# Kernel optimization log

Hardware: AMD Instinct MI355X
Metric: run time of the kernel (lower is better)

The kernel has to match this reference:

```python
import jax, jax.numpy as jnp
import numpy as np

B, S, H, KVH, D = 1, 2048, 32, 8, 128
ROPE_THETA = 500000.0


def _rotate_half(x):
    x1, x2 = jnp.split(x, 2, axis=-1)
    return jnp.concatenate((-x2, x1), axis=-1)


def setup_inputs() -> dict:
    key = jax.random.key(0)
    ks = jax.random.split(key, 5)
    hidden_states = jax.random.normal(ks[0], (B, S, H * D), dtype=jnp.float32)
    Wq = jax.random.normal(ks[1], (H * D, H * D), dtype=jnp.float32) * 0.02
    Wk = jax.random.normal(ks[2], (KVH * D, H * D), dtype=jnp.float32) * 0.02
    Wv = jax.random.normal(ks[3], (KVH * D, H * D), dtype=jnp.float32) * 0.02
    Wo = jax.random.normal(ks[4], (H * D, H * D), dtype=jnp.float32) * 0.02
    # rotary tables (Llama-style, concat of freqs with itself)
    inv_freq = 1.0 / (ROPE_THETA ** (jnp.arange(0, D, 2, dtype=jnp.float32) / D))
    freqs = jnp.arange(S, dtype=jnp.float32)[:, None] * inv_freq[None, :]  # [S, D/2]
    emb = jnp.concatenate((freqs, freqs), axis=-1)  # [S, D]
    cos = jnp.cos(emb)[None]  # [1, S, D]
    sin = jnp.sin(emb)[None]
    # additive causal mask, matching SDPA attn_mask semantics
    causal = jnp.tril(jnp.ones((S, S), dtype=bool))
    attention_mask = jnp.where(causal, 0.0, -1e9).astype(jnp.float32)[None, None]  # [1,1,S,S]
    return {"hidden_states": hidden_states, "attention_mask": attention_mask,
            "cos": cos, "sin": sin, "Wq": Wq, "Wk": Wk, "Wv": Wv, "Wo": Wo}


def reference(hidden_states, attention_mask, cos, sin, Wq, Wk, Wv, Wo):
    b, s, _ = hidden_states.shape
    d = cos.shape[-1]
    h = Wq.shape[0] // d
    kvh = Wk.shape[0] // d
    g = h // kvh  # GQA group size

    # fused QKV projection (nn.Linear: y = x @ W^T), then split heads -> [b, heads, s, d]
    q = jnp.einsum('bsi,oi->bso', hidden_states, Wq).reshape(b, s, h, d).transpose(0, 2, 1, 3)
    k = jnp.einsum('bsi,oi->bso', hidden_states, Wk).reshape(b, s, kvh, d).transpose(0, 2, 1, 3)
    v = jnp.einsum('bsi,oi->bso', hidden_states, Wv).reshape(b, s, kvh, d).transpose(0, 2, 1, 3)

    # rotary embedding (unsqueeze_dim=1)
    c = cos[:, None]  # [b,1,s,d]
    sn = sin[:, None]
    q = q * c + _rotate_half(q) * sn
    k = k * c + _rotate_half(k) * sn

    # GQA: view q as [b, kvh, g, s, d]; contract against un-repeated k/v
    qg = q.reshape(b, kvh, g, s, d)
    scale = 1.0 / jnp.sqrt(jnp.float32(d))
    scores = jnp.einsum('bkgsd,bktd->bkgst', qg, k) * scale  # [b,kvh,g,s,s]
    scores = scores + attention_mask[:, :, None]  # broadcast [b,1,1,s,s]
    probs = jax.nn.softmax(scores, axis=-1)
    attn = jnp.einsum('bkgst,bktd->bkgsd', probs, v)  # [b,kvh,g,s,d]

    attn = attn.reshape(b, h, s, d).transpose(0, 2, 1, 3).reshape(b, s, h * d)
    out = jnp.einsum('bso,po->bsp', attn, Wo)
    return out
```

## Files before the change

kernel.cpp:

```cpp
#include <hip/hip_runtime.h>
#include <hip/hip_bf16.h>

#define SEQ 2048
#define HD  128
#define NH  32
#define NKV 8
#define MODEL 4096
#define KVDIM 1024
#define QKVN 6144

typedef __attribute__((ext_vector_type(8))) short short8;
typedef __attribute__((ext_vector_type(4))) short short4v;
typedef __attribute__((ext_vector_type(4))) float float4v;

#define MFMA16(a, b, c) __builtin_amdgcn_mfma_f32_16x16x32_bf16(a, b, c, 0, 0, 0)

__device__ __forceinline__ short f2bf(float x) {
  unsigned u = __builtin_bit_cast(unsigned, x);
  u += 0x7fffu + ((u >> 16) & 1u);
  return (short)(u >> 16);
}
__device__ __forceinline__ float bf2f(short s) {
  unsigned u = ((unsigned)(unsigned short)s) << 16;
  return __builtin_bit_cast(float, u);
}

__device__ __forceinline__ void async_copy16(const void* g, void* l) {
  __builtin_amdgcn_global_load_lds((const __attribute__((address_space(1))) void*)g,
                                   (__attribute__((address_space(3))) void*)l, 16, 0, 0);
}

__global__ __launch_bounds__(256) void cast_fused(const float* __restrict__ wq,
                                                  const float* __restrict__ wk,
                                                  const float* __restrict__ wv,
                                                  const float* __restrict__ wo,
                                                  const float* __restrict__ hid,
                                                  short* __restrict__ dst) {
  int b = blockIdx.x;
  const float* src;
  int rbase, lblk;
  if (b < 16384)      { src = wq;  rbase = 0;     lblk = b; }
  else if (b < 20480) { src = wk;  rbase = 16384; lblk = b - 16384; }
  else if (b < 24576) { src = wv;  rbase = 20480; lblk = b - 20480; }
  else if (b < 40960) { src = wo;  rbase = 24576; lblk = b - 24576; }
  else                { src = hid; rbase = 40960; lblk = b - 40960; }
  size_t li = (size_t)lblk * 1024 + threadIdx.x * 4;
  float4v v = *(const float4v*)(src + li);
  short4v o;
  o[0] = f2bf(v[0]); o[1] = f2bf(v[1]); o[2] = f2bf(v[2]); o[3] = f2bf(v[3]);
  *(short4v*)(dst + (size_t)rbase * 1024 + li) = o;
}

__device__ __forceinline__ void store_out(float* C, size_t idx, float v) { C[idx] = v; }
__device__ __forceinline__ void store_out(short* C, size_t idx, float v) { C[idx] = f2bf(v); }

template <int NI, typename OUT>
__global__ __launch_bounds__(512, 2) void gemm256t(const short* __restrict__ A,
                                                   const short* __restrict__ B,
                                                   OUT* __restrict__ C,
                                                   int M, int N, int K) {
  constexpr int BN = NI * 64;
  __shared__ __align__(16) short As[2][256 * 64];
  __shared__ __align__(16) short Bs[2][BN * 64];
  const int tid = threadIdx.x;
  const int lane = tid & 63, w = tid >> 6;
  const int col = lane & 15, quad = lane >> 4;
  const int wm = w >> 2, wn = w & 3;

  const int nbx = N / BN;
  int bid = blockIdx.x, nwg = gridDim.x;
  int swz = (nwg & 7) ? bid : ((bid & 7) * (nwg >> 3) + (bid >> 3));
  const int m0 = (swz / nbx) << 8;
  const int n0 = (swz % nbx) * BN;

  const int srow = tid >> 3;
  const int schunk = (tid & 7) ^ (srow & 7);
  const short* pA = A + (size_t)(m0 + srow) * K + schunk * 8;
  const short* pB = B + (size_t)(n0 + srow) * K + schunk * 8;
  const int ldst = tid * 8;

  const int sw = (col & 7) << 3;
  const int kof0 = (quad * 8) ^ sw;
  const int kof1 = (32 + quad * 8) ^ sw;
  const int ra = wm * 128, rb = wn * (NI * 16);

  float4v acc[8][NI] = {};
  const int iters = K >> 6;

#define SA(buf, rA, kt) async_copy16(pA + (size_t)(rA) * K + (kt), &As[buf][(rA) * 64 + ldst])
#define SB_(buf, rB, kt) async_copy16(pB + (size_t)(rB) * K + (kt), &Bs[buf][(rB) * 64 + ldst])

  SA(0, 0, 0);  SA(0, 128, 0);
  SB_(0, 0, 0); SB_(0, 64, 0);
  if constexpr (NI == 3) SB_(0, 128, 0);
  SA(0, 64, 0); SA(0, 192, 0);
  asm volatile("s_waitcnt vmcnt(2)" ::: "memory");
  __builtin_amdgcn_s_barrier();

  for (int t = 0; t < iters; ++t) {
    const int cb = t & 1, nb = cb ^ 1;
    const int kt = (t + 1) << 6;
    const bool pf = (t + 1 < iters);
    const short* a_ = As[cb];
    const short* b_ = Bs[cb];
    short8 bf[NI][2];
    short8 af[4][2];

#pragma unroll
    for (int j = 0; j < 4; ++j) {
      const short* rp = a_ + (ra + j * 16 + col) * 64;
      af[j][0] = *(const short8*)(rp + kof0);
      af[j][1] = *(const short8*)(rp + kof1);
    }
#pragma unroll
    for (int ni = 0; ni < NI; ++ni) {
      const short* rp = b_ + (rb + ni * 16 + col) * 64;
      bf[ni][0] = *(const short8*)(rp + kof0);
      bf[ni][1] = *(const short8*)(rp + kof1);
    }
    if (pf) { SA(nb, 0, kt); SA(nb, 128, kt); SB_(nb, 0, kt); SB_(nb, 64, kt); }
    __builtin_amdgcn_s_barrier();
    asm volatile("s_waitcnt lgkmcnt(0)" ::: "memory");
    __builtin_amdgcn_sched_barrier(0);
    __builtin_amdgcn_s_setprio(1);
#pragma unroll
    for (int j = 0; j < 4; ++j)
#pragma unroll
      for (int ni = 0; ni < NI; ++ni) {
        acc[j][ni] = MFMA16(af[j][0], bf[ni][0], acc[j][ni]);
        acc[j][ni] = MFMA16(af[j][1], bf[ni][1], acc[j][ni]);
      }
    __builtin_amdgcn_s_setprio(0);
    if (pf) asm volatile("s_waitcnt vmcnt(4)" ::: "memory");
    else    asm volatile("s_waitcnt vmcnt(0)" ::: "memory");
    __builtin_amdgcn_s_barrier();

#pragma unroll
    for (int j = 0; j < 4; ++j) {
      const short* rp = a_ + (ra + (4 + j) * 16 + col) * 64;
      af[j][0] = *(const short8*)(rp + kof0);
      af[j][1] = *(const short8*)(rp + kof1);
    }
    if (pf) {
      if constexpr (NI == 3) SB_(nb, 128, kt);
      SA(nb, 64, kt); SA(nb, 192, kt);
    }
    __builtin_amdgcn_s_barrier();
    asm volatile("s_waitcnt lgkmcnt(0)" ::: "memory");
    __builtin_amdgcn_sched_barrier(0);
    __builtin_amdgcn_s_setprio(1);
#pragma unroll
    for (int j = 0; j < 4; ++j)
#pragma unroll
      for (int ni = 0; ni < NI; ++ni) {
        acc[4 + j][ni] = MFMA16(af[j][0], bf[ni][0], acc[4 + j][ni]);
        acc[4 + j][ni] = MFMA16(af[j][1], bf[ni][1], acc[4 + j][ni]);
      }
    __builtin_amdgcn_s_setprio(0);
    if (pf) asm volatile("s_waitcnt vmcnt(2)" ::: "memory");
    __builtin_amdgcn_s_barrier();
  }
#undef SA
#undef SB_

#pragma unroll
  for (int mi = 0; mi < 8; ++mi)
#pragma unroll
    for (int ni = 0; ni < NI; ++ni)
#pragma unroll
      for (int r = 0; r < 4; ++r) {
        int row = m0 + ra + mi * 16 + quad * 4 + r;
        int cc  = n0 + rb + ni * 16 + col;
        store_out(C, (size_t)row * N + cc, acc[mi][ni][r]);
      }
}

#define BM 128
#define BN 128
#define BK 32

template <typename OUT>
__global__ __launch_bounds__(256) void gemm_nt(const short* __restrict__ A,
                                               const short* __restrict__ B,
                                               OUT* __restrict__ C,
                                               int M, int N, int K) {
  __shared__ __align__(16) short As[2][BM * BK];
  __shared__ __align__(16) short Bs[2][BN * BK];
  int t = threadIdx.x;
  int w = t >> 6, lane = t & 63;
  int col = lane & 15, quad = lane >> 4;
  int m0 = blockIdx.y * BM, n0 = blockIdx.x * BN;
  int wr = (w >> 1) * 64, wc = (w & 1) * 64;

  int srow   = lane >> 2;
  int schunk = (lane & 3) ^ ((lane >> 3) & 3);
  const short* Ag0 = A + (size_t)(m0 + w * 32 + srow) * K + schunk * 8;
  const short* Ag1 = Ag0 + (size_t)16 * K;
  const short* Bg0 = B + (size_t)(n0 + w * 32 + srow) * K + schunk * 8;
  const short* Bg1 = Bg0 + (size_t)16 * K;
  const int wofs0 = (w * 32) * BK;
  const int wofs1 = (w * 32 + 16) * BK;

  int aswz = (quad ^ ((col >> 1) & 3)) * 8;

  float4v acc[4][4] = {};

  async_copy16(Ag0, &As[0][wofs0]);
  async_copy16(Ag1, &As[0][wofs1]);
  async_copy16(Bg0, &Bs[0][wofs0]);
  async_copy16(Bg1, &Bs[0][wofs1]);
  __syncthreads();

  const int iters = K / BK;
  for (int it = 0; it < iters; it++) {
    const int cb = it & 1, nb = cb ^ 1;
    if (it + 1 < iters) {
      const int k0 = (it + 1) * BK;
      async_copy16(Ag0 + k0, &As[nb][wofs0]);
      async_copy16(Ag1 + k0, &As[nb][wofs1]);
      async_copy16(Bg0 + k0, &Bs[nb][wofs0]);
      async_copy16(Bg1 + k0, &Bs[nb][wofs1]);
    }
    short8 af[4], bfr[4];
#pragma unroll
    for (int i = 0; i < 4; i++)
      af[i] = *(const short8*)&As[cb][(wr + i * 16 + col) * BK + aswz];
#pragma unroll
    for (int i = 0; i < 4; i++)
      bfr[i] = *(const short8*)&Bs[cb][(wc + i * 16 + col) * BK + aswz];
#pragma unroll
    for (int mi = 0; mi < 4; mi++)
#pragma unroll
      for (int ni = 0; ni < 4; ni++)
        acc[mi][ni] = MFMA16(af[mi], bfr[ni], acc[mi][ni]);
    __syncthreads();
  }

#pragma unroll
  for (int mi = 0; mi < 4; mi++)
#pragma unroll
    for (int ni = 0; ni < 4; ni++)
#pragma unroll
      for (int r = 0; r < 4; r++) {
        int row = m0 + wr + mi * 16 + quad * 4 + r;
        int cc  = n0 + wc + ni * 16 + col;
        store_out(C, (size_t)row * N + cc, acc[mi][ni][r]);
      }
}

__global__ __launch_bounds__(128) void rope_kernel(const short* __restrict__ qkv,
                                                   const float* __restrict__ cosp,
                                                   const float* __restrict__ sinp,
                                                   short* __restrict__ qb,
                                                   short* __restrict__ kb) {
  int s = blockIdx.x, head = blockIdx.y, d = threadIdx.x;
  float c  = cosp[s * HD + d];
  float sn = sinp[s * HD + d];
  if (head < NH) {
    const short* base = qkv + (size_t)s * QKVN + head * HD;
    float x = bf2f(base[d]);
    float rot = (d < 64) ? -bf2f(base[d + 64]) : bf2f(base[d - 64]);
    qb[((size_t)(head * SEQ + s)) * HD + d] = f2bf((x * c + rot * sn) * 0.08838834764831845f);
  } else {
    int hk = head - NH;
    const short* base = qkv + (size_t)s * QKVN + MODEL + hk * HD;
    float x = bf2f(base[d]);
    float rot = (d < 64) ? -bf2f(base[d + 64]) : bf2f(base[d - 64]);
    kb[((size_t)(hk * SEQ + s)) * HD + d] = f2bf(x * c + rot * sn);
  }
}

__global__ __launch_bounds__(256) void vtrans_kernel(const short* __restrict__ qkv,
                                                     short* __restrict__ vt) {
  __shared__ short tile[32][34];
  int kv = blockIdx.z;
  int d0 = blockIdx.x * 32, s0 = blockIdx.y * 32;
  int tx = threadIdx.x, ty = threadIdx.y;
#pragma unroll
  for (int j = 0; j < 32; j += 8)
    tile[ty + j][tx] = qkv[(size_t)(s0 + ty + j) * QKVN + MODEL + KVDIM + kv * HD + d0 + tx];
  __syncthreads();
#pragma unroll
  for (int j = 0; j < 32; j += 8)
    vt[((size_t)(kv * HD + d0 + ty + j)) * SEQ + s0 + tx] = tile[tx][ty + j];
}

#define FKT 32
#define KLD 136
#define VLD 40
#define PLD 40

__global__ __launch_bounds__(256, 3) void flash_attn(const short* __restrict__ qb_,
                                                     const short* __restrict__ kb,
                                                     const short* __restrict__ vt,
                                                     short* __restrict__ attn) {
  __shared__ __align__(16) short Ks[2][FKT * KLD];
  __shared__ __align__(16) short Vs[2][HD * VLD];
  __shared__ __align__(16) short Ps[4][32 * PLD];
  const int tid = threadIdx.x;
  const int w = tid >> 6, lane = tid & 63;
  const int col = lane & 15, quad = lane >> 4;
  const int h = blockIdx.x;
  const int kv = h >> 2;
  const int yp = (blockIdx.y < 8) ? (15 - (int)blockIdx.y) : ((int)blockIdx.y - 8);
  const int qB0 = yp * 128;
  const int q0w = qB0 + w * 32;
  const int ntiles = qB0 / FKT + 4;

  short8 ones;
#pragma unroll
  for (int i = 0; i < 8; i++) ones[i] = (short)0x3F80;

  short8 qf[2][4];
  const short* qbase = qb_ + ((size_t)(h * SEQ + q0w + col)) * HD;
#pragma unroll
  for (int rt = 0; rt < 2; rt++)
#pragma unroll
    for (int ks = 0; ks < 4; ks++)
      qf[rt][ks] = *(const short8*)(qbase + rt * 16 * HD + ks * 32 + quad * 8);

  float4v o[2][8] = {};
  float4v la[2] = {};

  const int kg_off = tid * 8;
  const int klds0  = (kg_off >> 7) * KLD + (kg_off & 127);
  const int vd     = tid >> 2;
  const int vkof   = (tid & 3) * 8;
  const size_t vrow0 = ((size_t)(kv * HD + vd)) * SEQ;
  const size_t vrow1 = ((size_t)(kv * HD + vd + 64)) * SEQ;
  const int vlds0 = vd * VLD + vkof;
  const short* kgbase = kb + ((size_t)kv * SEQ) * HD;

  short8 kr0, kr1, vr0, vr1;
  kr0 = *(const short8*)(kgbase + kg_off);
  kr1 = *(const short8*)(kgbase + 2048 + kg_off);
  vr0 = *(const short8*)(vt + vrow0 + vkof);
  vr1 = *(const short8*)(vt + vrow1 + vkof);
  *(short8*)&Ks[0][klds0]            = kr0;
  *(short8*)&Ks[0][klds0 + 16 * KLD] = kr1;
  *(short8*)&Vs[0][vlds0]            = vr0;
  *(short8*)&Vs[0][vlds0 + 64 * VLD] = vr1;
  __syncthreads();

  for (int kt = 0; kt < ntiles; kt++) {
    const int b = kt & 1;
    const int key0 = kt * FKT;
    if (kt + 1 < ntiles) {
      const int nk0 = key0 + FKT;
      const short* kg = kgbase + (size_t)nk0 * HD;
      kr0 = *(const short8*)(kg + kg_off);
      kr1 = *(const short8*)(kg + 2048 + kg_off);
      vr0 = *(const short8*)(vt + vrow0 + nk0 + vkof);
      vr1 = *(const short8*)(vt + vrow1 + nk0 + vkof);
    }
    if (key0 <= q0w + 31) {
      float4v sct[2][2] = {};
#pragma unroll
      for (int ks = 0; ks < 4; ks++) {
        short8 kf0 = *(const short8*)&Ks[b][col * KLD + ks * 32 + quad * 8];
        short8 kf1 = *(const short8*)&Ks[b][(16 + col) * KLD + ks * 32 + quad * 8];
        sct[0][0] = MFMA16(kf0, qf[0][ks], sct[0][0]);
        sct[0][1] = MFMA16(kf0, qf[1][ks], sct[0][1]);
        sct[1][0] = MFMA16(kf1, qf[0][ks], sct[1][0]);
        sct[1][1] = MFMA16(kf1, qf[1][ks], sct[1][1]);
      }
      short* pw = Ps[w];
#pragma unroll
      for (int rt = 0; rt < 2; rt++) {
        int qrow = q0w + rt * 16 + col;
#pragma unroll
        for (int kt2 = 0; kt2 < 2; kt2++) {
          int keyb = key0 + kt2 * 16 + quad * 4;
          short4v p;
#pragma unroll
          for (int r = 0; r < 4; r++) {
            float s = sct[kt2][rt][r];
            if (keyb + r > qrow) s = -INFINITY;
            p[r] = f2bf(__expf(s));
          }
          *(short4v*)&pw[(rt * 16 + col) * PLD + kt2 * 16 + quad * 4] = p;
        }
      }
      asm volatile("s_waitcnt lgkmcnt(0)" ::: "memory");
      short8 pf0 = *(const short8*)&pw[col * PLD + quad * 8];
      short8 pf1 = *(const short8*)&pw[(16 + col) * PLD + quad * 8];
      la[0] = MFMA16(ones, pf0, la[0]);
      la[1] = MFMA16(ones, pf1, la[1]);
#pragma unroll
      for (int nc = 0; nc < 8; nc++) {
        short8 vb = *(const short8*)&Vs[b][(nc * 16 + col) * VLD + quad * 8];
        o[0][nc] = MFMA16(vb, pf0, o[0][nc]);
        o[1][nc] = MFMA16(vb, pf1, o[1][nc]);
      }
    }
    if (kt + 1 < ntiles) {
      const int nb = 1 - b;
      *(short8*)&Ks[nb][klds0]            = kr0;
      *(short8*)&Ks[nb][klds0 + 16 * KLD] = kr1;
      *(short8*)&Vs[nb][vlds0]            = vr0;
      *(short8*)&Vs[nb][vlds0 + 64 * VLD] = vr1;
    }
    __syncthreads();
  }

#pragma unroll
  for (int rt = 0; rt < 2; rt++) {
    float inv = 1.0f / la[rt][0];
    size_t rowbase = (size_t)(q0w + rt * 16 + col) * MODEL + h * HD + quad * 4;
#pragma unroll
    for (int nc = 0; nc < 8; nc++) {
      short4v ov;
#pragma unroll
      for (int r = 0; r < 4; r++) ov[r] = f2bf(o[rt][nc][r] * inv);
      *(short4v*)(attn + rowbase + nc * 16) = ov;
    }
  }
}

extern "C" void kernel_launch(void* const* d_in, const int* in_sizes, int n_in,
                              void* d_out, int out_size, void* d_ws, size_t ws_size,
                              hipStream_t stream) {
  const float* hidden = (const float*)d_in[0];
  const float* cosp = (const float*)d_in[2];
  const float* sinp = (const float*)d_in[3];
  const float* Wq   = (const float*)d_in[4];
  const float* Wk   = (const float*)d_in[5];
  const float* Wv   = (const float*)d_in[6];
  const float* Wo   = (const float*)d_in[7];

  char* ws = (char*)d_ws;
  size_t off = 0;
  auto alloc = [&](size_t bytes) {
    char* p = ws + off;
    off += (bytes + 255) & ~(size_t)255;
    return p;
  };
  short* wq_bf = (short*)alloc((size_t)MODEL * MODEL * 2);
  short* wk_bf = (short*)alloc((size_t)KVDIM * MODEL * 2);
  short* wv_bf = (short*)alloc((size_t)KVDIM * MODEL * 2);
  short* wo_bf = (short*)alloc((size_t)MODEL * MODEL * 2);
  short* h_bf  = (short*)alloc((size_t)SEQ * MODEL * 2);
  short* qkv_bf = (short*)alloc((size_t)SEQ * QKVN * 2);
  short* k_bf  = (short*)alloc((size_t)NKV * SEQ * HD * 2);
  short* v_t   = (short*)alloc((size_t)NKV * HD * SEQ * 2);
  short* attn_bf = (short*)alloc((size_t)SEQ * MODEL * 2);
  short* q_bf    = h_bf;

  cast_fused<<<49152, 256, 0, stream>>>(Wq, Wk, Wv, Wo, hidden, wq_bf);

  gemm256t<3, short><<<dim3((SEQ / 256) * (QKVN / 192)), 512, 0, stream>>>(
      h_bf, wq_bf, qkv_bf, SEQ, QKVN, MODEL);

  rope_kernel<<<dim3(SEQ, NH + NKV), 128, 0, stream>>>(qkv_bf, cosp, sinp, q_bf, k_bf);
  vtrans_kernel<<<dim3(HD / 32, SEQ / 32, NKV), dim3(32, 8), 0, stream>>>(qkv_bf, v_t);

  flash_attn<<<dim3(NH, SEQ / 128), 256, 0, stream>>>(q_bf, k_bf, v_t, attn_bf);

  gemm_nt<float><<<dim3(MODEL / BN, SEQ / BM), 256, 0, stream>>>(
      attn_bf, wo_bf, (float*)d_out, SEQ, MODEL, MODEL);
}
```

Baseline: 518.7 us.

## Split GEMM k-step into four phases and fuse rope with V transpose

The QKV GEMM main loop now runs four MFMA phases of two row-tiles each instead of two phases of four. This spreads the async global prefetches across more barrier points and lowers register pressure for the A fragments, at the cost of extra barriers. Separately, the rope and V-transpose kernels are merged into one launch. The merged kernel uses 16-byte vectorized loads and stores for rotary and a wider shared-memory transpose, which cuts a launch and the scalar memory traffic.

```diff
diff --git a/kernel.cpp b/kernel.cpp
--- a/kernel.cpp
+++ b/kernel.cpp
@@ -55,7 +55,7 @@
 __device__ __forceinline__ void store_out(short* C, size_t idx, float v) { C[idx] = f2bf(v); }
 
 template <int NI, typename OUT>
-__global__ __launch_bounds__(512, 2) void gemm256t(const short* __restrict__ A,
+__global__ __launch_bounds__(512, 2) void gemm256v(const short* __restrict__ A,
                                                    const short* __restrict__ B,
                                                    OUT* __restrict__ C,
                                                    int M, int N, int K) {
@@ -104,10 +104,10 @@
     const short* a_ = As[cb];
     const short* b_ = Bs[cb];
     short8 bf[NI][2];
-    short8 af[4][2];
-
-#pragma unroll
-    for (int j = 0; j < 4; ++j) {
+    short8 af[2][2];
+
+#pragma unroll
+    for (int j = 0; j < 2; ++j) {
       const short* rp = a_ + (ra + j * 16 + col) * 64;
       af[j][0] = *(const short8*)(rp + kof0);
       af[j][1] = *(const short8*)(rp + kof1);
@@ -118,43 +118,82 @@
       bf[ni][0] = *(const short8*)(rp + kof0);
       bf[ni][1] = *(const short8*)(rp + kof1);
     }
-    if (pf) { SA(nb, 0, kt); SA(nb, 128, kt); SB_(nb, 0, kt); SB_(nb, 64, kt); }
+    if (pf) { SA(nb, 0, kt); SA(nb, 128, kt); }
     __builtin_amdgcn_s_barrier();
     asm volatile("s_waitcnt lgkmcnt(0)" ::: "memory");
     __builtin_amdgcn_sched_barrier(0);
     __builtin_amdgcn_s_setprio(1);
 #pragma unroll
-    for (int j = 0; j < 4; ++j)
+    for (int j = 0; j < 2; ++j)
 #pragma unroll
       for (int ni = 0; ni < NI; ++ni) {
         acc[j][ni] = MFMA16(af[j][0], bf[ni][0], acc[j][ni]);
         acc[j][ni] = MFMA16(af[j][1], bf[ni][1], acc[j][ni]);
       }
     __builtin_amdgcn_s_setprio(0);
+    __builtin_amdgcn_s_barrier();
+
+#pragma unroll
+    for (int j = 0; j < 2; ++j) {
+      const short* rp = a_ + (ra + (2 + j) * 16 + col) * 64;
+      af[j][0] = *(const short8*)(rp + kof0);
+      af[j][1] = *(const short8*)(rp + kof1);
+    }
+    if (pf) { SB_(nb, 0, kt); SB_(nb, 64, kt); }
+    __builtin_amdgcn_s_barrier();
+    asm volatile("s_waitcnt lgkmcnt(0)" ::: "memory");
+    __builtin_amdgcn_sched_barrier(0);
+    __builtin_amdgcn_s_setprio(1);
+#pragma unroll
+    for (int j = 0; j < 2; ++j)
+#pragma unroll
+      for (int ni = 0; ni < NI; ++ni) {
+        acc[2 + j][ni] = MFMA16(af[j][0], bf[ni][0], acc[2 + j][ni]);
+        acc[2 + j][ni] = MFMA16(af[j][1], bf[ni][1], acc[2 + j][ni]);
+      }
+    __builtin_amdgcn_s_setprio(0);
     if (pf) asm volatile("s_waitcnt vmcnt(4)" ::: "memory");
     else    asm volatile("s_waitcnt vmcnt(0)" ::: "memory");
     __builtin_amdgcn_s_barrier();
 
 #pragma unroll
-    for (int j = 0; j < 4; ++j) {
+    for (int j = 0; j < 2; ++j) {
       const short* rp = a_ + (ra + (4 + j) * 16 + col) * 64;
       af[j][0] = *(const short8*)(rp + kof0);
       af[j][1] = *(const short8*)(rp + kof1);
     }
-    if (pf) {
-      if constexpr (NI == 3) SB_(nb, 128, kt);
-      SA(nb, 64, kt); SA(nb, 192, kt);
-    }
+    if (pf) { if constexpr (NI == 3) SB_(nb, 128, kt); }
     __builtin_amdgcn_s_barrier();
     asm volatile("s_waitcnt lgkmcnt(0)" ::: "memory");
     __builtin_amdgcn_sched_barrier(0);
     __builtin_amdgcn_s_setprio(1);
 #pragma unroll
-    for (int j = 0; j < 4; ++j)
+    for (int j = 0; j < 2; ++j)
 #pragma unroll
       for (int ni = 0; ni < NI; ++ni) {
         acc[4 + j][ni] = MFMA16(af[j][0], bf[ni][0], acc[4 + j][ni]);
         acc[4 + j][ni] = MFMA16(af[j][1], bf[ni][1], acc[4 + j][ni]);
+      }
+    __builtin_amdgcn_s_setprio(0);
+    __builtin_amdgcn_s_barrier();
+
+#pragma unroll
+    for (int j = 0; j < 2; ++j) {
+      const short* rp = a_ + (ra + (6 + j) * 16 + col) * 64;
+      af[j][0] = *(const short8*)(rp + kof0);
+      af[j][1] = *(const short8*)(rp + kof1);
+    }
+    if (pf) { SA(nb, 64, kt); SA(nb, 192, kt); }
+    __builtin_amdgcn_s_barrier();
+    asm volatile("s_waitcnt lgkmcnt(0)" ::: "memory");
+    __builtin_amdgcn_sched_barrier(0);
+    __builtin_amdgcn_s_setprio(1);
+#pragma unroll
+    for (int j = 0; j < 2; ++j)
+#pragma unroll
+      for (int ni = 0; ni < NI; ++ni) {
+        acc[6 + j][ni] = MFMA16(af[j][0], bf[ni][0], acc[6 + j][ni]);
+        acc[6 + j][ni] = MFMA16(af[j][1], bf[ni][1], acc[6 + j][ni]);
       }
     __builtin_amdgcn_s_setprio(0);
     if (pf) asm volatile("s_waitcnt vmcnt(2)" ::: "memory");
@@ -248,41 +287,62 @@
       }
 }
 
-__global__ __launch_bounds__(128) void rope_kernel(const short* __restrict__ qkv,
-                                                   const float* __restrict__ cosp,
-                                                   const float* __restrict__ sinp,
-                                                   short* __restrict__ qb,
-                                                   short* __restrict__ kb) {
-  int s = blockIdx.x, head = blockIdx.y, d = threadIdx.x;
-  float c  = cosp[s * HD + d];
-  float sn = sinp[s * HD + d];
-  if (head < NH) {
-    const short* base = qkv + (size_t)s * QKVN + head * HD;
-    float x = bf2f(base[d]);
-    float rot = (d < 64) ? -bf2f(base[d + 64]) : bf2f(base[d - 64]);
-    qb[((size_t)(head * SEQ + s)) * HD + d] = f2bf((x * c + rot * sn) * 0.08838834764831845f);
+__global__ __launch_bounds__(256) void rope_fused(const short* __restrict__ qkv,
+                                                  const float* __restrict__ cosp,
+                                                  const float* __restrict__ sinp,
+                                                  short* __restrict__ qb,
+                                                  short* __restrict__ kb,
+                                                  short* __restrict__ vt) {
+  __shared__ short tile[32][137];
+  const int b = blockIdx.x, t = threadIdx.x;
+
+  if (b < 2560) {
+    const bool isq = b < 2048;
+    const int bb = isq ? b : b - 2048;
+    const int head = bb >> 6;
+    const int s = ((bb & 63) << 5) + (t >> 3);
+    const int d0 = (t & 7) * 8;
+    const int cbase = s * HD + d0;
+    float4v c0 = *(const float4v*)(cosp + cbase);
+    float4v c1 = *(const float4v*)(cosp + cbase + 4);
+    float4v s0v = *(const float4v*)(sinp + cbase);
+    float4v s1v = *(const float4v*)(sinp + cbase + 4);
+    const short* base = qkv + (size_t)s * QKVN + (isq ? head * HD : MODEL + head * HD) + d0;
+    short8 lo = *(const short8*)(base);
+    short8 hi = *(const short8*)(base + 64);
+    const float scale = isq ? 0.08838834764831845f : 1.0f;
+    short8 olo, ohi;
+#pragma unroll
+    for (int j = 0; j < 8; j++) {
+      float c = (j < 4) ? c0[j] : c1[j - 4];
+      float sn = (j < 4) ? s0v[j] : s1v[j - 4];
+      float l = bf2f(lo[j]), h = bf2f(hi[j]);
+      olo[j] = f2bf((l * c - h * sn) * scale);
+      ohi[j] = f2bf((h * c + l * sn) * scale);
+    }
+    short* out = (isq ? qb : kb) + ((size_t)(head * SEQ + s)) * HD + d0;
+    *(short8*)(out) = olo;
+    *(short8*)(out + 64) = ohi;
   } else {
-    int hk = head - NH;
-    const short* base = qkv + (size_t)s * QKVN + MODEL + hk * HD;
-    float x = bf2f(base[d]);
-    float rot = (d < 64) ? -bf2f(base[d + 64]) : bf2f(base[d - 64]);
-    kb[((size_t)(hk * SEQ + s)) * HD + d] = f2bf(x * c + rot * sn);
+    const int bb = b - 2560;
+    const int kv = bb >> 6;
+    const int s0 = (bb & 63) << 5;
+    const int lrow = t >> 4, chunk = t & 15;
+    const short* src = qkv + (size_t)(s0 + lrow) * QKVN + MODEL + KVDIM + kv * HD + chunk * 8;
+#pragma unroll
+    for (int rr = 0; rr < 2; rr++)
+      *(short8*)&tile[lrow + rr * 16][chunk * 8] =
+          *(const short8*)(src + (size_t)rr * 16 * QKVN);
+    __syncthreads();
+    const int sc = t & 3, d = t >> 2;
+#pragma unroll
+    for (int dd = 0; dd < 2; dd++) {
+      short8 o;
+#pragma unroll
+      for (int j = 0; j < 8; j++) o[j] = tile[sc * 8 + j][d + dd * 64];
+      *(short8*)(vt + ((size_t)(kv * HD + d + dd * 64)) * SEQ + s0 + sc * 8) = o;
+    }
   }
-}
-
-__global__ __launch_bounds__(256) void vtrans_kernel(const short* __restrict__ qkv,
-                                                     short* __restrict__ vt) {
-  __shared__ short tile[32][34];
-  int kv = blockIdx.z;
-  int d0 = blockIdx.x * 32, s0 = blockIdx.y * 32;
-  int tx = threadIdx.x, ty = threadIdx.y;
-#pragma unroll
-  for (int j = 0; j < 32; j += 8)
-    tile[ty + j][tx] = qkv[(size_t)(s0 + ty + j) * QKVN + MODEL + KVDIM + kv * HD + d0 + tx];
-  __syncthreads();
-#pragma unroll
-  for (int j = 0; j < 32; j += 8)
-    vt[((size_t)(kv * HD + d0 + ty + j)) * SEQ + s0 + tx] = tile[tx][ty + j];
 }
 
 #define FKT 32
@@ -448,11 +508,10 @@
 
   cast_fused<<<49152, 256, 0, stream>>>(Wq, Wk, Wv, Wo, hidden, wq_bf);
 
-  gemm256t<3, short><<<dim3((SEQ / 256) * (QKVN / 192)), 512, 0, stream>>>(
+  gemm256v<3, short><<<dim3((SEQ / 256) * (QKVN / 192)), 512, 0, stream>>>(
       h_bf, wq_bf, qkv_bf, SEQ, QKVN, MODEL);
 
-  rope_kernel<<<dim3(SEQ, NH + NKV), 128, 0, stream>>>(qkv_bf, cosp, sinp, q_bf, k_bf);
-  vtrans_kernel<<<dim3(HD / 32, SEQ / 32, NKV), dim3(32, 8), 0, stream>>>(qkv_bf, v_t);
+  rope_fused<<<3072, 256, 0, stream>>>(qkv_bf, cosp, sinp, q_bf, k_bf, v_t);
 
   flash_attn<<<dim3(NH, SEQ / 128), 256, 0, stream>>>(q_bf, k_bf, v_t, attn_bf);
 
```

After: 529.8 us. 2.1% more time.
